# Performance work log

Measured on AMD Instinct MI355X. Metric: run time of the kernel, lower is better.

Reference implementation:

```python
import jax, jax.numpy as jnp
import numpy as np

T, B, E, H = 2048, 2, 1024, 16
D = E // H
NEG = -1e18


def setup_inputs() -> dict:
    key = jax.random.key(0)
    k1, k2, k3, k4, k5 = jax.random.split(key, 5)
    return {
        "query": jax.random.normal(k1, (T, B, E), dtype=jnp.float32),
        "in_proj_weight": jax.random.normal(k2, (3 * E, E), dtype=jnp.float32) * 0.02,
        "in_proj_bias": jax.random.normal(k3, (3 * E,), dtype=jnp.float32) * 0.02,
        "out_proj_weight": jax.random.normal(k4, (E, E), dtype=jnp.float32) * 0.02,
        "out_proj_bias": jax.random.normal(k5, (E,), dtype=jnp.float32) * 0.02,
    }


def reference(query, in_proj_weight, in_proj_bias, out_proj_weight, out_proj_bias):
    # Self-attention (qkv_same), mask_future_timesteps=True, no padding mask,
    # eval mode (dropout p=0), need_weights=True.
    tgt_len, bsz, embed_dim = query.shape
    # fused in-projection: [T,B,3E]
    qkv = jnp.einsum("tbe,fe->tbf", query, in_proj_weight) + in_proj_bias
    q, k, v = jnp.split(qkv, 3, axis=-1)
    q = q * (D ** -0.5)
    # [T,B,E] -> [B*H, T, D]
    def to_heads(x):
        return x.reshape(tgt_len, bsz * H, D).transpose(1, 0, 2)
    q, k, v = to_heads(q), to_heads(k), to_heads(v)
    # scores: [B*H, T, T]
    scores = jnp.einsum("ntd,nsd->nts", q, k)
    causal = jnp.triu(jnp.full((tgt_len, tgt_len), NEG, dtype=scores.dtype), k=1)
    scores = scores + causal[None, :, :]
    attn_weights = jax.nn.softmax(scores, axis=-1)
    # context: [B*H, T, D] -> [T, B, E]
    ctx = jnp.einsum("nts,nsd->ntd", attn_weights, v)
    ctx = ctx.transpose(1, 0, 2).reshape(tgt_len, bsz, embed_dim)
    out = jnp.einsum("tbe,fe->tbf", ctx, out_proj_weight) + out_proj_bias
    # averaged attention weights over heads: [B, T, T]
    avg_w = attn_weights.reshape(bsz, H, tgt_len, tgt_len).sum(axis=1) / H
    return (out, avg_w)
```

## Files before the change

kernel.cpp:

```cpp
#include <hip/hip_runtime.h>
#include <math.h>

#define T_LEN 2048
#define BSZ 2
#define EMB 1024
#define NHEAD 16
#define HDIM 64
#define QK_LD 2048

typedef __attribute__((ext_vector_type(8))) short short8v;
typedef __attribute__((ext_vector_type(4))) float floatx4;

__device__ __forceinline__ short f2bf(float f) {
    unsigned u = __float_as_uint(f);
    u += 0x7fffu + ((u >> 16) & 1u);
    return (short)(u >> 16);
}

__global__ __launch_bounds__(256) void f32_to_bf16_k(const float* __restrict__ src,
                                                     short* __restrict__ dst, int n) {
    int i = (blockIdx.x * 256 + threadIdx.x) * 4;
    if (i >= n) return;
    float4 v = *(const float4*)(src + i);
    short4 o = make_short4(f2bf(v.x), f2bf(v.y), f2bf(v.z), f2bf(v.w));
    *(short4*)(dst + i) = o;
}

__global__ __launch_bounds__(256) void gemm_bf16(const void* __restrict__ Ain,
        const short* __restrict__ B, const float* __restrict__ bias,
        void* __restrict__ Cout, short* __restrict__ vTout,
        int M, int N, int K, int scale_cols, int out_bf16, int ldC, int a_fp32) {
    __shared__ short As[128][32];
    __shared__ short Bs[128][32];
    const int tid = threadIdx.x;
    const int m0 = blockIdx.x * 128, n0 = blockIdx.y * 128;
    const int lane = tid & 63, w = tid >> 6;
    const int q = lane >> 4, r = lane & 15;
    const int wr = w >> 1, wc = w & 1;
    const int srow = tid >> 2, sc4 = tid & 3;
    const int sp = (sc4 ^ ((srow >> 1) & 3)) * 8;

    const short* Brow0 = B + (size_t)(n0 + srow) * K + sc4 * 8;
    const short* Brow1 = Brow0 + (size_t)64 * K;

    floatx4 acc[4][4];
    #pragma unroll
    for (int a = 0; a < 4; ++a)
        #pragma unroll
        for (int b2 = 0; b2 < 4; ++b2)
            #pragma unroll
            for (int e = 0; e < 4; ++e) acc[a][b2][e] = 0.f;

    for (int k0 = 0; k0 < K; k0 += 32) {
        int4 a0, a1;
        if (a_fp32) {
            const float* Af = (const float*)Ain;
            const float* p0 = Af + (size_t)(m0 + srow) * K + sc4 * 8 + k0;
            const float* p1 = p0 + (size_t)64 * K;
            float4 f00 = *(const float4*)p0, f01 = *(const float4*)(p0 + 4);
            float4 f10 = *(const float4*)p1, f11 = *(const float4*)(p1 + 4);
            short4 s00 = make_short4(f2bf(f00.x), f2bf(f00.y), f2bf(f00.z), f2bf(f00.w));
            short4 s01 = make_short4(f2bf(f01.x), f2bf(f01.y), f2bf(f01.z), f2bf(f01.w));
            short4 s10 = make_short4(f2bf(f10.x), f2bf(f10.y), f2bf(f10.z), f2bf(f10.w));
            short4 s11 = make_short4(f2bf(f11.x), f2bf(f11.y), f2bf(f11.z), f2bf(f11.w));
            a0 = make_int4(*(int*)&s00.x, *(int*)&s00.z, *(int*)&s01.x, *(int*)&s01.z);
            a1 = make_int4(*(int*)&s10.x, *(int*)&s10.z, *(int*)&s11.x, *(int*)&s11.z);
        } else {
            const short* As8 = (const short*)Ain + (size_t)(m0 + srow) * K + sc4 * 8 + k0;
            a0 = *(const int4*)As8;
            a1 = *(const int4*)(As8 + (size_t)64 * K);
        }
        int4 b0 = *(const int4*)(Brow0 + k0);
        int4 b1 = *(const int4*)(Brow1 + k0);
        __syncthreads();
        *(int4*)&As[srow][sp] = a0;
        *(int4*)&As[64 + srow][sp] = a1;
        *(int4*)&Bs[srow][sp] = b0;
        *(int4*)&Bs[64 + srow][sp] = b1;
        __syncthreads();
        short8v af[4], bfr[4];
        #pragma unroll
        for (int mb = 0; mb < 4; ++mb) {
            int row = wr * 64 + mb * 16 + r;
            af[mb] = *(const short8v*)&As[row][(q ^ ((row >> 1) & 3)) * 8];
        }
        #pragma unroll
        for (int nb = 0; nb < 4; ++nb) {
            int row = wc * 64 + nb * 16 + r;
            bfr[nb] = *(const short8v*)&Bs[row][(q ^ ((row >> 1) & 3)) * 8];
        }
        #pragma unroll
        for (int mb = 0; mb < 4; ++mb)
            #pragma unroll
            for (int nb = 0; nb < 4; ++nb)
                acc[mb][nb] = __builtin_amdgcn_mfma_f32_16x16x32_bf16(af[mb], bfr[nb], acc[mb][nb], 0, 0, 0);
    }

    #pragma unroll
    for (int nb = 0; nb < 4; ++nb) {
        const int col = n0 + wc * 64 + nb * 16 + r;
        const float bi = bias[col];
        const float sc = (col < scale_cols) ? 0.125f : 1.0f;
        if (vTout && col >= 2 * EMB) {
            const int e = col - 2 * EMB;
            #pragma unroll
            for (int mb = 0; mb < 4; ++mb) {
                const int base = m0 + wr * 64 + mb * 16 + q * 4;
                float v0 = acc[mb][nb][0] + bi, v1 = acc[mb][nb][1] + bi;
                float v2 = acc[mb][nb][2] + bi, v3 = acc[mb][nb][3] + bi;
                unsigned lo = (unsigned short)f2bf(v0) | ((unsigned)(unsigned short)f2bf(v2) << 16);
                unsigned hi = (unsigned short)f2bf(v1) | ((unsigned)(unsigned short)f2bf(v3) << 16);
                *(unsigned*)&vTout[(size_t)e * T_LEN + (base >> 1)]         = lo;
                *(unsigned*)&vTout[((size_t)EMB + e) * T_LEN + (base >> 1)] = hi;
            }
        } else {
            #pragma unroll
            for (int mb = 0; mb < 4; ++mb)
                #pragma unroll
                for (int i = 0; i < 4; ++i) {
                    const int rowg = m0 + wr * 64 + mb * 16 + q * 4 + i;
                    const float v = (acc[mb][nb][i] + bi) * sc;
                    if (out_bf16) ((short*)Cout)[(size_t)rowg * ldC + col] = f2bf(v);
                    else          ((float*)Cout)[(size_t)rowg * ldC + col] = v;
                }
        }
    }
}

__global__ __launch_bounds__(256) void flash_fwd(const short* __restrict__ qk,
        const short* __restrict__ vT, short* __restrict__ ctx,
        float* __restrict__ Lr) {
    __shared__ short Ks[128][64];
    __shared__ short Vt[64][128];
    __shared__ short Ps[2][64][64];
    __shared__ float Lred[4][64];
    const int tid = threadIdx.x;
    const int bh = blockIdx.x;
    const int pairi = blockIdx.y;
    const int b = bh >> 4, h = bh & 15;
    const int lane = tid & 63, w = tid >> 6;
    const int q = lane >> 4, r = lane & 15;
    const int RS = BSZ * QK_LD;

    const short* qbase = qk + (size_t)b * QK_LD + h * HDIM;
    const short* kbase = qbase + EMB;
    const short* vbase = vT + ((size_t)b * EMB + h * HDIM) * T_LEN;

    for (int pass = 0; pass < 2; ++pass) {
        const int tt = pass ? (31 - pairi) : pairi;
        const int t0 = tt << 6;
        __syncthreads();
        {
            const int sr = tid >> 3, c8 = tid & 7;
            *(int4*)&Ps[0][sr][(c8 ^ (sr & 7)) * 8] =
                *(const int4*)(qbase + (size_t)(t0 + sr) * RS + c8 * 8);
            *(int4*)&Ps[0][sr + 32][(c8 ^ ((sr + 32) & 7)) * 8] =
                *(const int4*)(qbase + (size_t)(t0 + sr + 32) * RS + c8 * 8);
        }
        __syncthreads();
        short8v qf[4][2];
        #pragma unroll
        for (int mb = 0; mb < 4; ++mb)
            #pragma unroll
            for (int ks = 0; ks < 2; ++ks) {
                int row = mb * 16 + r;
                qf[mb][ks] = *(const short8v*)&Ps[0][row][((ks * 4 + q) ^ (row & 7)) * 8];
            }

        float l_part[4][4];
        floatx4 o[4];
        #pragma unroll
        for (int mb = 0; mb < 4; ++mb)
            #pragma unroll
            for (int i = 0; i < 4; ++i) l_part[mb][i] = 0.f;
        #pragma unroll
        for (int nb = 0; nb < 4; ++nb)
            #pragma unroll
            for (int e = 0; e < 4; ++e) o[nb][e] = 0.f;

        const int ntiles = tt + 1;
        int s2 = 0;
        for (; s2 + 2 <= ntiles; s2 += 2) {
            __syncthreads();
            {
                const int sr = tid >> 1, cb = (tid & 1) * 4;
                const short* kp = kbase + (size_t)(s2 * 64 + sr) * RS;
                #pragma unroll
                for (int u = 0; u < 4; ++u) {
                    const int c = cb + u;
                    *(int4*)&Ks[sr][(c ^ (sr & 7)) * 8] = *(const int4*)(kp + c * 8);
                }
                const int vr = tid >> 2, vb0 = (tid & 3) * 4;
                const short* vp = vbase + (size_t)vr * T_LEN + s2 * 64;
                #pragma unroll
                for (int u = 0; u < 4; ++u) {
                    const int c = vb0 + u;
                    const int pc = (c & 8) | ((c & 7) ^ (vr & 7));
                    *(int4*)&Vt[vr][pc * 8] = *(const int4*)(vp + c * 8);
                }
            }
            __syncthreads();
            #pragma unroll
            for (int t2 = 0; t2 < 2; ++t2) {
                floatx4 sf[4];
                #pragma unroll
                for (int mb = 0; mb < 4; ++mb)
                    #pragma unroll
                    for (int e = 0; e < 4; ++e) sf[mb][e] = 0.f;
                #pragma unroll
                for (int ks = 0; ks < 2; ++ks) {
                    const int krow = t2 * 64 + w * 16 + r;
                    short8v kf = *(const short8v*)&Ks[krow][((ks * 4 + q) ^ (krow & 7)) * 8];
                    #pragma unroll
                    for (int mb = 0; mb < 4; ++mb)
                        sf[mb] = __builtin_amdgcn_mfma_f32_16x16x32_bf16(qf[mb][ks], kf, sf[mb], 0, 0, 0);
                }
                const bool diag = (s2 + t2 == tt);
                #pragma unroll
                for (int mb = 0; mb < 4; ++mb)
                    #pragma unroll
                    for (int i = 0; i < 4; ++i) {
                        const int rl = mb * 16 + q * 4 + i;
                        float p = (diag && (w * 16 + r > rl)) ? 0.f : __expf(sf[mb][i]);
                        l_part[mb][i] += p;
                        const int c = (w * 2 + (r >> 3)) ^ (rl & 7);
                        Ps[t2][rl][c * 8 + (r & 7)] = f2bf(p);
                    }
            }
            __syncthreads();
            #pragma unroll
            for (int ks = 0; ks < 2; ++ks) {
                const int prow = w * 16 + r;
                const int pcp = ((ks * 4 + q) ^ (prow & 7)) * 8;
                short8v pfA = *(const short8v*)&Ps[0][prow][pcp];
                short8v pfB = *(const short8v*)&Ps[1][prow][pcp];
                #pragma unroll
                for (int nb = 0; nb < 4; ++nb) {
                    const int vrow = nb * 16 + r;
                    const int pcv = (ks * 4 + q) ^ (vrow & 7);
                    short8v vfA = *(const short8v*)&Vt[vrow][pcv * 8];
                    short8v vfB = *(const short8v*)&Vt[vrow][(8 | pcv) * 8];
                    o[nb] = __builtin_amdgcn_mfma_f32_16x16x32_bf16(pfA, vfA, o[nb], 0, 0, 0);
                    o[nb] = __builtin_amdgcn_mfma_f32_16x16x32_bf16(pfB, vfB, o[nb], 0, 0, 0);
                }
            }
        }
        if (s2 < ntiles) {
            __syncthreads();
            {
                const int sr = tid >> 2, cb = (tid & 3) * 2;
                const short* kp = kbase + (size_t)(s2 * 64 + sr) * RS;
                const short* vp = vbase + (size_t)sr * T_LEN + s2 * 64;
                #pragma unroll
                for (int u = 0; u < 2; ++u) {
                    const int c = cb + u;
                    *(int4*)&Ks[sr][(c ^ (sr & 7)) * 8] = *(const int4*)(kp + c * 8);
                    *(int4*)&Vt[sr][(c ^ (sr & 7)) * 8] = *(const int4*)(vp + c * 8);
                }
            }
            __syncthreads();
            floatx4 sf[4];
            #pragma unroll
            for (int mb = 0; mb < 4; ++mb)
                #pragma unroll
                for (int e = 0; e < 4; ++e) sf[mb][e] = 0.f;
            #pragma unroll
            for (int ks = 0; ks < 2; ++ks) {
                const int krow = w * 16 + r;
                short8v kf = *(const short8v*)&Ks[krow][((ks * 4 + q) ^ (krow & 7)) * 8];
                #pragma unroll
                for (int mb = 0; mb < 4; ++mb)
                    sf[mb] = __builtin_amdgcn_mfma_f32_16x16x32_bf16(qf[mb][ks], kf, sf[mb], 0, 0, 0);
            }
            #pragma unroll
            for (int mb = 0; mb < 4; ++mb)
                #pragma unroll
                for (int i = 0; i < 4; ++i) {
                    const int rl = mb * 16 + q * 4 + i;
                    float p = (w * 16 + r > rl) ? 0.f : __expf(sf[mb][i]);
                    l_part[mb][i] += p;
                    const int c = (w * 2 + (r >> 3)) ^ (rl & 7);
                    Ps[0][rl][c * 8 + (r & 7)] = f2bf(p);
                }
            __syncthreads();
            #pragma unroll
            for (int ks = 0; ks < 2; ++ks) {
                const int prow = w * 16 + r;
                short8v pf = *(const short8v*)&Ps[0][prow][((ks * 4 + q) ^ (prow & 7)) * 8];
                #pragma unroll
                for (int nb = 0; nb < 4; ++nb) {
                    const int vrow = nb * 16 + r;
                    short8v vf = *(const short8v*)&Vt[vrow][(((ks * 4 + q) ^ (vrow & 7))) * 8];
                    o[nb] = __builtin_amdgcn_mfma_f32_16x16x32_bf16(pf, vf, o[nb], 0, 0, 0);
                }
            }
        }

        #pragma unroll
        for (int mb = 0; mb < 4; ++mb)
            #pragma unroll
            for (int i = 0; i < 4; ++i) {
                float v = l_part[mb][i];
                v += __shfl_xor(v, 1, 16);
                v += __shfl_xor(v, 2, 16);
                v += __shfl_xor(v, 4, 16);
                v += __shfl_xor(v, 8, 16);
                if (r == 0) Lred[w][mb * 16 + q * 4 + i] = v;
            }
        __syncthreads();
        if (tid < 64) {
            float s = Lred[0][tid] + Lred[1][tid] + Lred[2][tid] + Lred[3][tid];
            Lr[(size_t)bh * T_LEN + t0 + tid] = s;
            Lred[0][tid] = s;
        }
        __syncthreads();
        #pragma unroll
        for (int i = 0; i < 4; ++i) {
            const int tl = w * 16 + q * 4 + i;
            const float inv = 1.0f / Lred[0][tl];
            #pragma unroll
            for (int nb = 0; nb < 4; ++nb)
                ctx[((size_t)(t0 + tl) * BSZ + b) * EMB + h * HDIM + nb * 16 + r] =
                    f2bf(o[nb][i] * inv);
        }
    }
}

__global__ __launch_bounds__(256) void avg_w_k(const short* __restrict__ qk,
        const float* __restrict__ Lr, float* __restrict__ avg) {
    const int s0 = blockIdx.x * 64, t0 = blockIdx.y * 64, b = blockIdx.z;
    const int tid = threadIdx.x;
    float* outb = avg + (size_t)b * T_LEN * T_LEN;
    if (s0 > t0) {
        const int ty = tid >> 4, tx = tid & 15;
        const float4 z = make_float4(0.f, 0.f, 0.f, 0.f);
        #pragma unroll
        for (int i = 0; i < 4; ++i)
            *(float4*)&outb[(size_t)(t0 + ty * 4 + i) * T_LEN + s0 + tx * 4] = z;
        return;
    }
    __shared__ short Qs[64][128];
    __shared__ short Ks[64][128];
    __shared__ float Lbuf[NHEAD][64];
    const int lane = tid & 63, w = tid >> 6;
    const int q = lane >> 4, r = lane & 15;
    const int srow = tid >> 2, c4 = (tid & 3) * 4;
    const short* qbase = qk + (size_t)b * QK_LD;
    const int RS = BSZ * QK_LD;

    #pragma unroll
    for (int u = 0; u < 4; ++u) {
        const int li = tid * 4 + u;
        const int h = li >> 6, tl = li & 63;
        Lbuf[h][tl] = 0.0625f / Lr[(size_t)(b * NHEAD + h) * T_LEN + t0 + tl];
    }

    floatx4 acc[4];
    #pragma unroll
    for (int nb = 0; nb < 4; ++nb)
        #pragma unroll
        for (int e = 0; e < 4; ++e) acc[nb][e] = 0.f;

    for (int hp = 0; hp < 8; ++hp) {
        const short* qh = qbase + hp * 128;
        const short* kh = qbase + EMB + hp * 128;
        __syncthreads();
        #pragma unroll
        for (int u = 0; u < 4; ++u) {
            const int c = c4 + u;
            const int pc = (c & 8) | ((c & 7) ^ (srow & 7));
            *(int4*)&Qs[srow][pc * 8] =
                *(const int4*)(qh + (size_t)(t0 + srow) * RS + c * 8);
            *(int4*)&Ks[srow][pc * 8] =
                *(const int4*)(kh + (size_t)(s0 + srow) * RS + c * 8);
        }
        __syncthreads();

        #pragma unroll
        for (int hs = 0; hs < 2; ++hs) {
            const int h = hp * 2 + hs;
            floatx4 sf[4];
            #pragma unroll
            for (int nb = 0; nb < 4; ++nb)
                #pragma unroll
                for (int e = 0; e < 4; ++e) sf[nb][e] = 0.f;
            #pragma unroll
            for (int ks = 0; ks < 2; ++ks) {
                const int qrow = w * 16 + r;
                short8v qfr = *(const short8v*)
                    &Qs[qrow][((hs * 8) | ((ks * 4 + q) ^ (qrow & 7))) * 8];
                #pragma unroll
                for (int nb = 0; nb < 4; ++nb) {
                    const int krow = nb * 16 + r;
                    short8v kfr = *(const short8v*)
                        &Ks[krow][((hs * 8) | ((ks * 4 + q) ^ (krow & 7))) * 8];
                    sf[nb] = __builtin_amdgcn_mfma_f32_16x16x32_bf16(qfr, kfr, sf[nb], 0, 0, 0);
                }
            }
            #pragma unroll
            for (int i = 0; i < 4; ++i) {
                const int tl = w * 16 + q * 4 + i;
                const float inv = Lbuf[h][tl];
                #pragma unroll
                for (int nb = 0; nb < 4; ++nb) {
                    float e = (s0 == t0 && (nb * 16 + r > tl))
                              ? 0.f : __expf(sf[nb][i]) * inv;
                    acc[nb][i] += e;
                }
            }
        }
    }

    #pragma unroll
    for (int i = 0; i < 4; ++i) {
        const int t = t0 + w * 16 + q * 4 + i;
        #pragma unroll
        for (int nb = 0; nb < 4; ++nb)
            outb[(size_t)t * T_LEN + s0 + nb * 16 + r] = acc[nb][i];
    }
}

extern "C" void kernel_launch(void* const* d_in, const int* in_sizes, int n_in,
                              void* d_out, int out_size, void* d_ws, size_t ws_size,
                              hipStream_t stream) {
    (void)in_sizes; (void)n_in; (void)out_size; (void)ws_size;
    const float* query = (const float*)d_in[0];
    const float* w_in  = (const float*)d_in[1];
    const float* b_in  = (const float*)d_in[2];
    const float* w_out = (const float*)d_in[3];
    const float* b_out = (const float*)d_in[4];

    float* out = (float*)d_out;
    float* avg = out + (size_t)T_LEN * BSZ * EMB;

    short* ws     = (short*)d_ws;
    short* wb_in  = ws;
    short* wb_out = wb_in  + (size_t)3072 * 1024;
    short* qkb    = wb_out + (size_t)1024 * 1024;
    short* vTb    = qkb    + (size_t)4096 * 2048;
    short* ctxb   = vTb    + (size_t)BSZ * EMB * T_LEN;
    float* Lr     = (float*)(ctxb + (size_t)4096 * 1024);

    f32_to_bf16_k<<<3072, 256, 0, stream>>>(w_in,  wb_in,  3072 * 1024);
    f32_to_bf16_k<<<1024, 256, 0, stream>>>(w_out, wb_out, 1024 * 1024);

    gemm_bf16<<<dim3(32, 24), 256, 0, stream>>>(query, wb_in, b_in, qkb, vTb,
                                                4096, 3072, 1024, EMB, 1, QK_LD, 1);
    flash_fwd<<<dim3(32, 16), 256, 0, stream>>>(qkb, vTb, ctxb, Lr);
    avg_w_k<<<dim3(32, 32, 2), 256, 0, stream>>>(qkb, Lr, avg);
    gemm_bf16<<<dim3(32, 8), 256, 0, stream>>>(ctxb, wb_out, b_out, out, (short*)0,
                                               4096, 1024, 1024, 0, 0, 1024, 0);
}
```

Baseline: 256.6 us.

## Use direct global-to-LDS async loads in bf16 GEMM and pre-convert query

The GEMM tile loads now use global_load_lds, which writes 16-byte chunks straight into shared memory. The XOR swizzle is applied on the source-address side, so data no longer passes through registers and no explicit LDS stores are needed. To make this possible, the fp32 query is first converted to bf16 in a separate kernel that writes into the ctx buffer, and the in-kernel fp32-to-bf16 conversion path is removed. This adds an extra kernel launch and one more round trip of the query through memory. The loop is still single-buffered, so load latency is not overlapped with compute.

```diff
diff --git a/kernel.cpp b/kernel.cpp
--- a/kernel.cpp
+++ b/kernel.cpp
@@ -15,6 +15,12 @@
     unsigned u = __float_as_uint(f);
     u += 0x7fffu + ((u >> 16) & 1u);
     return (short)(u >> 16);
+}
+
+__device__ __forceinline__ void async16(const short* g, short* l) {
+    __builtin_amdgcn_global_load_lds(
+        (const __attribute__((address_space(1))) void*)g,
+        (__attribute__((address_space(3))) void*)l, 16, 0, 0);
 }
 
 __global__ __launch_bounds__(256) void f32_to_bf16_k(const float* __restrict__ src,
@@ -26,10 +32,10 @@
     *(short4*)(dst + i) = o;
 }
 
-__global__ __launch_bounds__(256) void gemm_bf16(const void* __restrict__ Ain,
+__global__ __launch_bounds__(256) void gemm_bf16(const short* __restrict__ A,
         const short* __restrict__ B, const float* __restrict__ bias,
         void* __restrict__ Cout, short* __restrict__ vTout,
-        int M, int N, int K, int scale_cols, int out_bf16, int ldC, int a_fp32) {
+        int M, int N, int K, int scale_cols, int out_bf16, int ldC) {
     __shared__ short As[128][32];
     __shared__ short Bs[128][32];
     const int tid = threadIdx.x;
@@ -37,11 +43,20 @@
     const int lane = tid & 63, w = tid >> 6;
     const int q = lane >> 4, r = lane & 15;
     const int wr = w >> 1, wc = w & 1;
-    const int srow = tid >> 2, sc4 = tid & 3;
-    const int sp = (sc4 ^ ((srow >> 1) & 3)) * 8;
-
-    const short* Brow0 = B + (size_t)(n0 + srow) * K + sc4 * 8;
-    const short* Brow1 = Brow0 + (size_t)64 * K;
+
+    const int srow = lane >> 2;
+    const int spos = lane & 3;
+    const int rowL = w * 16 + srow;
+    const int rowH = 64 + rowL;
+    const int csrc = spos ^ ((rowL >> 1) & 3);
+    const short* gA0 = A + (size_t)(m0 + rowL) * K + csrc * 8;
+    const short* gA1 = A + (size_t)(m0 + rowH) * K + csrc * 8;
+    const short* gB0 = B + (size_t)(n0 + rowL) * K + csrc * 8;
+    const short* gB1 = B + (size_t)(n0 + rowH) * K + csrc * 8;
+    short* lA0 = &As[w * 16][0];
+    short* lA1 = &As[64 + w * 16][0];
+    short* lB0 = &Bs[w * 16][0];
+    short* lB1 = &Bs[64 + w * 16][0];
 
     floatx4 acc[4][4];
     #pragma unroll
@@ -52,31 +67,11 @@
             for (int e = 0; e < 4; ++e) acc[a][b2][e] = 0.f;
 
     for (int k0 = 0; k0 < K; k0 += 32) {
-        int4 a0, a1;
-        if (a_fp32) {
-            const float* Af = (const float*)Ain;
-            const float* p0 = Af + (size_t)(m0 + srow) * K + sc4 * 8 + k0;
-            const float* p1 = p0 + (size_t)64 * K;
-            float4 f00 = *(const float4*)p0, f01 = *(const float4*)(p0 + 4);
-            float4 f10 = *(const float4*)p1, f11 = *(const float4*)(p1 + 4);
-            short4 s00 = make_short4(f2bf(f00.x), f2bf(f00.y), f2bf(f00.z), f2bf(f00.w));
-            short4 s01 = make_short4(f2bf(f01.x), f2bf(f01.y), f2bf(f01.z), f2bf(f01.w));
-            short4 s10 = make_short4(f2bf(f10.x), f2bf(f10.y), f2bf(f10.z), f2bf(f10.w));
-            short4 s11 = make_short4(f2bf(f11.x), f2bf(f11.y), f2bf(f11.z), f2bf(f11.w));
-            a0 = make_int4(*(int*)&s00.x, *(int*)&s00.z, *(int*)&s01.x, *(int*)&s01.z);
-            a1 = make_int4(*(int*)&s10.x, *(int*)&s10.z, *(int*)&s11.x, *(int*)&s11.z);
-        } else {
-            const short* As8 = (const short*)Ain + (size_t)(m0 + srow) * K + sc4 * 8 + k0;
-            a0 = *(const int4*)As8;
-            a1 = *(const int4*)(As8 + (size_t)64 * K);
-        }
-        int4 b0 = *(const int4*)(Brow0 + k0);
-        int4 b1 = *(const int4*)(Brow1 + k0);
-        __syncthreads();
-        *(int4*)&As[srow][sp] = a0;
-        *(int4*)&As[64 + srow][sp] = a1;
-        *(int4*)&Bs[srow][sp] = b0;
-        *(int4*)&Bs[64 + srow][sp] = b1;
+        __syncthreads();
+        async16(gA0 + k0, lA0);
+        async16(gA1 + k0, lA1);
+        async16(gB0 + k0, lB0);
+        async16(gB1 + k0, lB1);
         __syncthreads();
         short8v af[4], bfr[4];
         #pragma unroll
@@ -440,14 +435,16 @@
     short* vTb    = qkb    + (size_t)4096 * 2048;
     short* ctxb   = vTb    + (size_t)BSZ * EMB * T_LEN;
     float* Lr     = (float*)(ctxb + (size_t)4096 * 1024);
-
+    short* qb     = ctxb;
+
+    f32_to_bf16_k<<<4096, 256, 0, stream>>>(query, qb,     4096 * 1024);
     f32_to_bf16_k<<<3072, 256, 0, stream>>>(w_in,  wb_in,  3072 * 1024);
     f32_to_bf16_k<<<1024, 256, 0, stream>>>(w_out, wb_out, 1024 * 1024);
 
-    gemm_bf16<<<dim3(32, 24), 256, 0, stream>>>(query, wb_in, b_in, qkb, vTb,
-                                                4096, 3072, 1024, EMB, 1, QK_LD, 1);
+    gemm_bf16<<<dim3(32, 24), 256, 0, stream>>>(qb, wb_in, b_in, qkb, vTb,
+                                                4096, 3072, 1024, EMB, 1, QK_LD);
     flash_fwd<<<dim3(32, 16), 256, 0, stream>>>(qkb, vTb, ctxb, Lr);
     avg_w_k<<<dim3(32, 32, 2), 256, 0, stream>>>(qkb, Lr, avg);
     gemm_bf16<<<dim3(32, 8), 256, 0, stream>>>(ctxb, wb_out, b_out, out, (short*)0,
-                                               4096, 1024, 1024, 0, 0, 1024, 0);
-}
+                                               4096, 1024, 1024, 0, 0, 1024);
+}
```

After: 250.8 us. 1.02x faster.
